# Kernel tuning notes

Hardware: AMD Instinct MI355X
Metric: run time of the kernel (lower is better)

The kernel has to match this reference:

```python
import jax, jax.numpy as jnp
import numpy as np

BASE_ALPHA = 0.1
NUM_ITER = 4


def setup_inputs() -> dict:
    key = jax.random.key(0)
    k1, k2 = jax.random.split(key)
    pred = jax.random.normal(k1, (8, 8192, 3), dtype=jnp.float32)
    partial = jax.random.normal(k2, (8, 2048, 3), dtype=jnp.float32)
    return {"pred": pred, "partial": partial}


def _pairwise_dist(x, y):
    x2 = jnp.sum(x * x, axis=-1)[..., :, None]          # [B, N, 1]
    y2 = jnp.sum(y * y, axis=-1)[..., None, :]          # [B, 1, M]
    xy = jnp.einsum('bnd,bmd->bnm', x, y)               # [B, N, M]
    return jnp.sqrt(jnp.maximum(x2 + y2 - 2.0 * xy, 0.0))


def reference(pred, partial):
    refined = pred
    for _ in range(NUM_ITER):
        dist = _pairwise_dist(refined, partial)          # [B, N, M]
        min_dist = jnp.min(dist, axis=-1)                # [B, N]
        min_idx = jnp.argmin(dist, axis=-1)              # [B, N]
        nearest = jnp.take_along_axis(partial, min_idx[..., None], axis=1)  # [B, N, 3]
        dist_norm = min_dist / (jnp.max(min_dist, axis=-1, keepdims=True) + 1e-6)
        alpha = BASE_ALPHA * (2.0 - dist_norm)           # [B, N]
        refined = refined + alpha[..., None] * (nearest - refined)
    return refined
```

## Files before the change

kernel.cpp:

```cpp
#include <hip/hip_runtime.h>

#define B 8
#define N 8192
#define M 2048
#define NITER 4
#define BASE_ALPHA 0.1f
#define MARGIN 0.02f
#define CAP 16

#define NTHR 1024
#define NPT 32
#define NSPLIT 32
#define JS (M / NSPLIT)
#define JQ (JS / 4)
#define PT 8
#define PPB (NPT * PT)
#define NBLK (B * N / PPB)

#define LTHR 256
#define BPB 32

#define OFF_AUX   (1024 * 1024)
#define OFF_MASK  (1536 * 1024)
#define OFF_CNT   (1792 * 1024)
#define OFF_CANDL (2048 * 1024)
#define OFF_SLOT0 (4096 * 1024)
#define OFF_SLOT1 (4100 * 1024)

typedef float f2 __attribute__((ext_vector_type(2)));

__global__ __launch_bounds__(NTHR, 4) void iter_kernel(const float* __restrict__ pred,
                                                       const float* __restrict__ partial,
                                                       float4* __restrict__ pos4,
                                                       uint2* __restrict__ aux,
                                                       unsigned int* __restrict__ maskbuf,
                                                       unsigned int* __restrict__ gcnt,
                                                       unsigned short* __restrict__ gcand,
                                                       float* __restrict__ slots) {
    __shared__ float4 sX[M / 4], sY[M / 4], sZ[M / 4], sW[M / 4];
    __shared__ float smint[NSPLIT][PPB];
    __shared__ float4 lpos[PPB];
    __shared__ float thrsh[PPB];
    __shared__ unsigned int smask[PPB];
    __shared__ float redbuf[4];

    const int tid = threadIdx.x;
    const int b = blockIdx.x >> 5;
    const int blk = blockIdx.x & 31;
    const int gp0 = b * N + blk * PPB;

    const float* pa = partial + b * M * 3;
    if (tid < M / 4) {
        int sp = tid & 31, jq = tid >> 5;
        const float* p0 = pa + (sp * JS + jq * 4) * 3;
        float a0 = p0[0], a1 = p0[1],  a2 = p0[2];
        float b0 = p0[3], b1 = p0[4],  b2 = p0[5];
        float c0 = p0[6], c1 = p0[7],  c2 = p0[8];
        float d0 = p0[9], d1 = p0[10], d2 = p0[11];
        sX[tid] = make_float4(-2.f * a0, -2.f * b0, -2.f * c0, -2.f * d0);
        sY[tid] = make_float4(-2.f * a1, -2.f * b1, -2.f * c1, -2.f * d1);
        sZ[tid] = make_float4(-2.f * a2, -2.f * b2, -2.f * c2, -2.f * d2);
        sW[tid] = make_float4(a0 * a0 + a1 * a1 + a2 * a2, b0 * b0 + b1 * b1 + b2 * b2,
                              c0 * c0 + c1 * c1 + c2 * c2, d0 * d0 + d1 * d1 + d2 * d2);
    }

    if (tid < PPB) {
        const int p = gp0 + tid;
        const float* pp = pred + (unsigned long long)p * 3;
        float rx = pp[0], ry = pp[1], rz = pp[2];
        float w = rx * rx + ry * ry + rz * rz;
        lpos[tid] = make_float4(rx, ry, rz, w);
        pos4[p] = make_float4(rx, ry, rz, w);
    }
    __syncthreads();

    const int split = tid >> 5;
    const int pt = tid & 31;

    f2 sx[PT], sy[PT], sz[PT];
    #pragma unroll
    for (int k = 0; k < PT; ++k) {
        float4 r = lpos[pt + k * NPT];
        sx[k] = (f2){r.x, r.x}; sy[k] = (f2){r.y, r.y}; sz[k] = (f2){r.z, r.z};
    }
    f2 acc[PT];
    #pragma unroll
    for (int k = 0; k < PT; ++k) acc[k] = (f2){3.402823466e+38f, 3.402823466e+38f};

    #pragma unroll 2
    for (int jq = 0; jq < JQ; ++jq) {
        float4 qx = sX[jq * 32 + split], qy = sY[jq * 32 + split];
        float4 qz = sZ[jq * 32 + split], qw = sW[jq * 32 + split];
        f2 qx01 = (f2){qx.x, qx.y}, qx23 = (f2){qx.z, qx.w};
        f2 qy01 = (f2){qy.x, qy.y}, qy23 = (f2){qy.z, qy.w};
        f2 qz01 = (f2){qz.x, qz.y}, qz23 = (f2){qz.z, qz.w};
        f2 qw01 = (f2){qw.x, qw.y}, qw23 = (f2){qw.z, qw.w};
        #pragma unroll
        for (int k = 0; k < PT; ++k) {
            f2 t01 = __builtin_elementwise_fma(sx[k], qx01,
                     __builtin_elementwise_fma(sy[k], qy01,
                     __builtin_elementwise_fma(sz[k], qz01, qw01)));
            f2 t23 = __builtin_elementwise_fma(sx[k], qx23,
                     __builtin_elementwise_fma(sy[k], qy23,
                     __builtin_elementwise_fma(sz[k], qz23, qw23)));
            acc[k] = __builtin_elementwise_min(acc[k],
                     __builtin_elementwise_min(t01, t23));
        }
    }
    #pragma unroll
    for (int k = 0; k < PT; ++k)
        smint[split][pt + k * NPT] = fminf(acc[k].x, acc[k].y);
    __syncthreads();

    if (tid < PPB) {
        float tstar = 3.402823466e+38f; int bsplit = 0;
        #pragma unroll
        for (int s = 0; s < NSPLIT; ++s) {
            float v = smint[s][tid];
            if (v < tstar) { tstar = v; bsplit = s; }
        }
        const float4 f4 = lpos[tid];
        const float md = sqrtf(fmaxf(f4.w + tstar, 0.0f));
        float mdm = md + MARGIN;
        float thr = fmaf(mdm, mdm, -f4.w);
        thrsh[tid] = thr;
        unsigned int mask = 0u;
        #pragma unroll
        for (int s = 0; s < NSPLIT; ++s)
            if (smint[s][tid] <= thr) mask |= (1u << s);
        smask[tid] = mask;
        maskbuf[gp0 + tid] = mask;

        float bt = 3.402823466e+38f; int bj = 0;
        for (int jq = 0; jq < JQ; ++jq) {
            float4 qx = sX[jq * 32 + bsplit], qy = sY[jq * 32 + bsplit];
            float4 qz = sZ[jq * 32 + bsplit], qw = sW[jq * 32 + bsplit];
            float t0 = fmaf(f4.x, qx.x, fmaf(f4.y, qy.x, fmaf(f4.z, qz.x, qw.x)));
            float t1 = fmaf(f4.x, qx.y, fmaf(f4.y, qy.y, fmaf(f4.z, qz.y, qw.y)));
            float t2 = fmaf(f4.x, qx.z, fmaf(f4.y, qy.z, fmaf(f4.z, qz.z, qw.z)));
            float t3 = fmaf(f4.x, qx.w, fmaf(f4.y, qy.w, fmaf(f4.z, qz.w, qw.w)));
            if (t0 < bt) { bt = t0; bj = jq * 4 + 0; }
            if (t1 < bt) { bt = t1; bj = jq * 4 + 1; }
            if (t2 < bt) { bt = t2; bj = jq * 4 + 2; }
            if (t3 < bt) { bt = t3; bj = jq * 4 + 3; }
        }
        aux[gp0 + tid] = make_uint2(__float_as_uint(md),
                                    (unsigned int)(bsplit * JS + bj));

        float wm = md;
        #pragma unroll
        for (int o = 32; o > 0; o >>= 1) wm = fmaxf(wm, __shfl_down(wm, o));
        if ((tid & 63) == 0) redbuf[tid >> 6] = wm;
    }
    __syncthreads();
    if (tid == 0)
        slots[b * BPB + blk] = fmaxf(fmaxf(redbuf[0], redbuf[1]),
                                     fmaxf(redbuf[2], redbuf[3]));

    {
        const int lane = tid & 63;
        const int wv = tid >> 6;
        const unsigned long long lmask = (1ull << lane) - 1ull;
        const int jq2 = lane >> 2, c2 = lane & 3;
        for (int q0 = 0; q0 < 16; ++q0) {
            int q = wv * 16 + q0;
            float4 f4 = lpos[q];
            float thr = thrsh[q];
            unsigned int m = smask[q];
            int cnt = 0;
            unsigned long long cb = (unsigned long long)(gp0 + q) * CAP;
            while (m) {
                int s = __builtin_ctz(m); m &= m - 1;
                int e = (jq2 * 32 + s) * 4 + c2;
                float qx = ((const float*)sX)[e];
                float qy = ((const float*)sY)[e];
                float qz = ((const float*)sZ)[e];
                float qw = ((const float*)sW)[e];
                float t = fmaf(f4.x, qx, fmaf(f4.y, qy, fmaf(f4.z, qz, qw)));
                bool hit = (t <= thr);
                unsigned long long bal = __ballot(hit);
                int pos = cnt + (int)__popcll(bal & lmask);
                if (hit && pos < CAP)
                    gcand[cb + pos] = (unsigned short)(s * JS + lane);
                cnt += (int)__popcll(bal);
            }
            if (lane == 0) gcnt[gp0 + q] = (unsigned int)cnt;
        }
    }
}

__device__ __attribute__((noinline)) void nn_fallback(float x, float y, float z,
                                                      unsigned int mk,
                                                      const float* __restrict__ pa,
                                                      float& bt_out, int& bj_out) {
    float bt = 3.402823466e+38f; int bj = 0;
    unsigned int m = mk;
    while (m) {
        int s = __builtin_ctz(m); m &= m - 1;
        int jb = s * JS;
        for (int jj = 0; jj < JS; ++jj) {
            int j = jb + jj;
            const float* py = pa + j * 3;
            float y0 = py[0], y1 = py[1], y2 = py[2];
            float qx = -2.f * y0, qy = -2.f * y1, qz = -2.f * y2;
            float qw = y0 * y0 + y1 * y1 + y2 * y2;
            float t = fmaf(x, qx, fmaf(y, qy, fmaf(z, qz, qw)));
            if (t < bt) { bt = t; bj = j; }
        }
    }
    bt_out = bt; bj_out = bj;
}

__global__ __launch_bounds__(LTHR) void light_kernel(const float* __restrict__ partial,
                                                     float4* __restrict__ pos4,
                                                     uint2* __restrict__ aux,
                                                     const unsigned int* __restrict__ maskbuf,
                                                     const unsigned int* __restrict__ gcnt,
                                                     const unsigned short* __restrict__ gcand,
                                                     const float* __restrict__ slots_in,
                                                     float* __restrict__ slots_out) {
    __shared__ float redbuf[4];
    __shared__ float mxsh;

    const int tid = threadIdx.x;
    const int p = blockIdx.x * LTHR + tid;
    const int b = p >> 13;
    const int blk = blockIdx.x & 31;
    const float* pa = partial + b * M * 3;

    if (tid < 64) {
        float v = slots_in[b * BPB + (tid & 31)];
        #pragma unroll
        for (int o = 16; o > 0; o >>= 1) v = fmaxf(v, __shfl_xor(v, o));
        if (tid == 0) mxsh = v;
    }
    __syncthreads();

    float4 f = pos4[p];
    uint2 a = aux[p];
    float md = __uint_as_float(a.x);
    unsigned int cnt = gcnt[p];

    const float* py = pa + (int)a.y * 3;
    float y0 = py[0], y1 = py[1], y2 = py[2];
    float inv = 1.0f / (mxsh + 1e-6f);
    float alpha = BASE_ALPHA * (2.0f - md * inv);
    float nx = fmaf(alpha, y0 - f.x, f.x);
    float ny = fmaf(alpha, y1 - f.y, f.y);
    float nz = fmaf(alpha, y2 - f.z, f.z);
    float w = nx * nx + ny * ny + nz * nz;
    pos4[p] = make_float4(nx, ny, nz, w);

    float bt = 3.402823466e+38f; int bj = 0;
    if (cnt <= CAP) {
        const unsigned short* cp = gcand + (unsigned long long)p * CAP;
        for (unsigned int c = 0; c < cnt; ++c) {
            int j = cp[c];
            const float* pj = pa + j * 3;
            float a0 = pj[0], a1 = pj[1], a2 = pj[2];
            float qx = -2.f * a0, qy = -2.f * a1, qz = -2.f * a2;
            float qw = a0 * a0 + a1 * a1 + a2 * a2;
            float t = fmaf(nx, qx, fmaf(ny, qy, fmaf(nz, qz, qw)));
            if (t < bt || (t == bt && j < bj)) { bt = t; bj = j; }
        }
    } else {
        nn_fallback(nx, ny, nz, maskbuf[p], pa, bt, bj);
    }
    float mdn = sqrtf(fmaxf(w + bt, 0.0f));
    aux[p] = make_uint2(__float_as_uint(mdn), (unsigned int)bj);

    float wm = mdn;
    #pragma unroll
    for (int o = 32; o > 0; o >>= 1) wm = fmaxf(wm, __shfl_down(wm, o));
    if ((tid & 63) == 0) redbuf[tid >> 6] = wm;
    __syncthreads();
    if (tid == 0)
        slots_out[b * BPB + blk] = fmaxf(fmaxf(redbuf[0], redbuf[1]),
                                         fmaxf(redbuf[2], redbuf[3]));
}

__global__ __launch_bounds__(LTHR) void final_kernel(const float* __restrict__ partial,
                                                     const float4* __restrict__ pos4,
                                                     const uint2* __restrict__ aux,
                                                     const float* __restrict__ slots,
                                                     float* __restrict__ out) {
    __shared__ float mxsh;
    const int p = blockIdx.x * LTHR + threadIdx.x;
    const int b = p >> 13;
    if (threadIdx.x < 64) {
        float v = slots[b * BPB + (threadIdx.x & 31)];
        #pragma unroll
        for (int o = 16; o > 0; o >>= 1) v = fmaxf(v, __shfl_xor(v, o));
        if (threadIdx.x == 0) mxsh = v;
    }
    __syncthreads();
    float4 f = pos4[p];
    uint2 a = aux[p];
    float md = __uint_as_float(a.x);
    const float* py = partial + ((unsigned long long)(b * M + (int)a.y)) * 3;
    float y0 = py[0], y1 = py[1], y2 = py[2];
    float inv = 1.0f / (mxsh + 1e-6f);
    float alpha = BASE_ALPHA * (2.0f - md * inv);
    float* po = out + (unsigned long long)p * 3;
    po[0] = fmaf(alpha, y0 - f.x, f.x);
    po[1] = fmaf(alpha, y1 - f.y, f.y);
    po[2] = fmaf(alpha, y2 - f.z, f.z);
}

extern "C" void kernel_launch(void* const* d_in, const int* in_sizes, int n_in,
                              void* d_out, int out_size, void* d_ws, size_t ws_size,
                              hipStream_t stream) {
    const float* pred = (const float*)d_in[0];
    const float* partial = (const float*)d_in[1];
    char* ws = (char*)d_ws;
    float4* pos4 = (float4*)ws;
    uint2* aux = (uint2*)(ws + OFF_AUX);
    unsigned int* maskb = (unsigned int*)(ws + OFF_MASK);
    unsigned int* gcnt = (unsigned int*)(ws + OFF_CNT);
    unsigned short* gcand = (unsigned short*)(ws + OFF_CANDL);
    float* slot0 = (float*)(ws + OFF_SLOT0);
    float* slot1 = (float*)(ws + OFF_SLOT1);
    float* out = (float*)d_out;

    hipLaunchKernelGGL(iter_kernel, dim3(NBLK), dim3(NTHR), 0, stream,
                       pred, partial, pos4, aux, maskb, gcnt, gcand, slot0);
    hipLaunchKernelGGL(light_kernel, dim3(B * N / LTHR), dim3(LTHR), 0, stream,
                       partial, pos4, aux, maskb, gcnt, gcand, slot0, slot1);
    hipLaunchKernelGGL(light_kernel, dim3(B * N / LTHR), dim3(LTHR), 0, stream,
                       partial, pos4, aux, maskb, gcnt, gcand, slot1, slot0);
    hipLaunchKernelGGL(light_kernel, dim3(B * N / LTHR), dim3(LTHR), 0, stream,
                       partial, pos4, aux, maskb, gcnt, gcand, slot0, slot1);
    hipLaunchKernelGGL(final_kernel, dim3(B * N / LTHR), dim3(LTHR), 0, stream,
                       partial, pos4, aux, slot1, out);
}
```

Baseline: 98.20 us.

## Fuse exact argmin into wave-parallel candidate scan and tighten margin

Removes the serial per-thread 64-point argmin over the best split and instead computes the exact nearest neighbour inside the wave-parallel candidate scan, using a warp shuffle reduction with index tie-breaking. Adds an AoS shared copy of the partial points so each lane does one float4 LDS read. Lowers the pruning margin to shrink candidate masks, and adds an extra barrier plus a per-point md buffer for the block max reduction. The smaller margin could change which splits get scanned, and the extra LDS may reduce occupancy.

```diff
diff --git a/kernel.cpp b/kernel.cpp
--- a/kernel.cpp
+++ b/kernel.cpp
@@ -5,7 +5,7 @@
 #define M 2048
 #define NITER 4
 #define BASE_ALPHA 0.1f
-#define MARGIN 0.02f
+#define MARGIN 0.005f
 #define CAP 16
 
 #define NTHR 1024
@@ -38,10 +38,12 @@
                                                        unsigned short* __restrict__ gcand,
                                                        float* __restrict__ slots) {
     __shared__ float4 sX[M / 4], sY[M / 4], sZ[M / 4], sW[M / 4];
+    __shared__ float4 sC[M];
     __shared__ float smint[NSPLIT][PPB];
     __shared__ float4 lpos[PPB];
     __shared__ float thrsh[PPB];
     __shared__ unsigned int smask[PPB];
+    __shared__ float pmd[PPB];
     __shared__ float redbuf[4];
 
     const int tid = threadIdx.x;
@@ -57,11 +59,19 @@
         float b0 = p0[3], b1 = p0[4],  b2 = p0[5];
         float c0 = p0[6], c1 = p0[7],  c2 = p0[8];
         float d0 = p0[9], d1 = p0[10], d2 = p0[11];
+        float wa = a0 * a0 + a1 * a1 + a2 * a2;
+        float wb = b0 * b0 + b1 * b1 + b2 * b2;
+        float wc = c0 * c0 + c1 * c1 + c2 * c2;
+        float wd = d0 * d0 + d1 * d1 + d2 * d2;
         sX[tid] = make_float4(-2.f * a0, -2.f * b0, -2.f * c0, -2.f * d0);
         sY[tid] = make_float4(-2.f * a1, -2.f * b1, -2.f * c1, -2.f * d1);
         sZ[tid] = make_float4(-2.f * a2, -2.f * b2, -2.f * c2, -2.f * d2);
-        sW[tid] = make_float4(a0 * a0 + a1 * a1 + a2 * a2, b0 * b0 + b1 * b1 + b2 * b2,
-                              c0 * c0 + c1 * c1 + c2 * c2, d0 * d0 + d1 * d1 + d2 * d2);
+        sW[tid] = make_float4(wa, wb, wc, wd);
+        int j0 = sp * JS + jq * 4;
+        sC[j0 + 0] = make_float4(-2.f * a0, -2.f * a1, -2.f * a2, wa);
+        sC[j0 + 1] = make_float4(-2.f * b0, -2.f * b1, -2.f * b2, wb);
+        sC[j0 + 2] = make_float4(-2.f * c0, -2.f * c1, -2.f * c2, wc);
+        sC[j0 + 3] = make_float4(-2.f * d0, -2.f * d1, -2.f * d2, wd);
     }
 
     if (tid < PPB) {
@@ -113,12 +123,9 @@
     __syncthreads();
 
     if (tid < PPB) {
-        float tstar = 3.402823466e+38f; int bsplit = 0;
-        #pragma unroll
-        for (int s = 0; s < NSPLIT; ++s) {
-            float v = smint[s][tid];
-            if (v < tstar) { tstar = v; bsplit = s; }
-        }
+        float tstar = 3.402823466e+38f;
+        #pragma unroll
+        for (int s = 0; s < NSPLIT; ++s) tstar = fminf(tstar, smint[s][tid]);
         const float4 f4 = lpos[tid];
         const float md = sqrtf(fmaxf(f4.w + tstar, 0.0f));
         float mdm = md + MARGIN;
@@ -130,38 +137,13 @@
             if (smint[s][tid] <= thr) mask |= (1u << s);
         smask[tid] = mask;
         maskbuf[gp0 + tid] = mask;
-
-        float bt = 3.402823466e+38f; int bj = 0;
-        for (int jq = 0; jq < JQ; ++jq) {
-            float4 qx = sX[jq * 32 + bsplit], qy = sY[jq * 32 + bsplit];
-            float4 qz = sZ[jq * 32 + bsplit], qw = sW[jq * 32 + bsplit];
-            float t0 = fmaf(f4.x, qx.x, fmaf(f4.y, qy.x, fmaf(f4.z, qz.x, qw.x)));
-            float t1 = fmaf(f4.x, qx.y, fmaf(f4.y, qy.y, fmaf(f4.z, qz.y, qw.y)));
-            float t2 = fmaf(f4.x, qx.z, fmaf(f4.y, qy.z, fmaf(f4.z, qz.z, qw.z)));
-            float t3 = fmaf(f4.x, qx.w, fmaf(f4.y, qy.w, fmaf(f4.z, qz.w, qw.w)));
-            if (t0 < bt) { bt = t0; bj = jq * 4 + 0; }
-            if (t1 < bt) { bt = t1; bj = jq * 4 + 1; }
-            if (t2 < bt) { bt = t2; bj = jq * 4 + 2; }
-            if (t3 < bt) { bt = t3; bj = jq * 4 + 3; }
-        }
-        aux[gp0 + tid] = make_uint2(__float_as_uint(md),
-                                    (unsigned int)(bsplit * JS + bj));
-
-        float wm = md;
-        #pragma unroll
-        for (int o = 32; o > 0; o >>= 1) wm = fmaxf(wm, __shfl_down(wm, o));
-        if ((tid & 63) == 0) redbuf[tid >> 6] = wm;
-    }
-    __syncthreads();
-    if (tid == 0)
-        slots[b * BPB + blk] = fmaxf(fmaxf(redbuf[0], redbuf[1]),
-                                     fmaxf(redbuf[2], redbuf[3]));
+    }
+    __syncthreads();
 
     {
         const int lane = tid & 63;
         const int wv = tid >> 6;
         const unsigned long long lmask = (1ull << lane) - 1ull;
-        const int jq2 = lane >> 2, c2 = lane & 3;
         for (int q0 = 0; q0 < 16; ++q0) {
             int q = wv * 16 + q0;
             float4 f4 = lpos[q];
@@ -169,24 +151,46 @@
             unsigned int m = smask[q];
             int cnt = 0;
             unsigned long long cb = (unsigned long long)(gp0 + q) * CAP;
+            float bt = 3.402823466e+38f; int bj = 0;
             while (m) {
                 int s = __builtin_ctz(m); m &= m - 1;
-                int e = (jq2 * 32 + s) * 4 + c2;
-                float qx = ((const float*)sX)[e];
-                float qy = ((const float*)sY)[e];
-                float qz = ((const float*)sZ)[e];
-                float qw = ((const float*)sW)[e];
-                float t = fmaf(f4.x, qx, fmaf(f4.y, qy, fmaf(f4.z, qz, qw)));
+                int j = s * JS + lane;
+                float4 c = sC[j];
+                float t = fmaf(f4.x, c.x, fmaf(f4.y, c.y, fmaf(f4.z, c.z, c.w)));
+                if (t < bt) { bt = t; bj = j; }
                 bool hit = (t <= thr);
                 unsigned long long bal = __ballot(hit);
                 int pos = cnt + (int)__popcll(bal & lmask);
                 if (hit && pos < CAP)
-                    gcand[cb + pos] = (unsigned short)(s * JS + lane);
+                    gcand[cb + pos] = (unsigned short)j;
                 cnt += (int)__popcll(bal);
             }
-            if (lane == 0) gcnt[gp0 + q] = (unsigned int)cnt;
+            #pragma unroll
+            for (int o = 32; o > 0; o >>= 1) {
+                float to = __shfl_xor(bt, o);
+                int jo = __shfl_xor(bj, o);
+                if (to < bt || (to == bt && jo < bj)) { bt = to; bj = jo; }
+            }
+            if (lane == 0) {
+                gcnt[gp0 + q] = (unsigned int)cnt;
+                float md = sqrtf(fmaxf(f4.w + bt, 0.0f));
+                aux[gp0 + q] = make_uint2(__float_as_uint(md), (unsigned int)bj);
+                pmd[q] = md;
+            }
         }
     }
+    __syncthreads();
+
+    if (tid < PPB) {
+        float wm = pmd[tid];
+        #pragma unroll
+        for (int o = 32; o > 0; o >>= 1) wm = fmaxf(wm, __shfl_down(wm, o));
+        if ((tid & 63) == 0) redbuf[tid >> 6] = wm;
+    }
+    __syncthreads();
+    if (tid == 0)
+        slots[b * BPB + blk] = fmaxf(fmaxf(redbuf[0], redbuf[1]),
+                                     fmaxf(redbuf[2], redbuf[3]));
 }
 
 __device__ __attribute__((noinline)) void nn_fallback(float x, float y, float z,
```

Measured after the change: 99.85 us. No clear change (+1.7%).
